# Kernel optimization log

Measured on AMD Instinct MI355X. Metric: run time of the kernel, lower is better.

## Reference

```python
import jax, jax.numpy as jnp
import numpy as np

D = 1024
B = 16
T = 2048
LN_EPS = 1e-5


def setup_inputs() -> dict:
    key = jax.random.key(0)
    k_x, k_in, k_st = jax.random.split(key, 3)
    x = jax.random.normal(k_x, (B, T, D), dtype=jnp.float32)
    # nn.Linear(d, 2d, bias=False): weight [2D, D], y = x @ W.T
    s_in = 1.0 / np.sqrt(D)
    W_in = jax.random.uniform(k_in, (2 * D, D), dtype=jnp.float32, minval=-s_in, maxval=s_in)
    W_state = jax.random.uniform(k_st, (D, D), dtype=jnp.float32, minval=-s_in, maxval=s_in)
    gamma = jnp.ones((D,), dtype=jnp.float32)
    beta = jnp.zeros((D,), dtype=jnp.float32)
    return {"x": x, "W_in": W_in, "W_state": W_state, "gamma": gamma, "beta": beta}


def _glru(x, W_in, W_state, gamma, beta):
    # Batched projections over all timesteps (gates depend only on x).
    proj = jnp.einsum("btd,ed->bte", x, W_in)            # [B, T, 2D]
    gx, vx = jnp.split(proj, 2, axis=-1)                   # each [B, T, D]
    u = jax.nn.sigmoid(gx)                                  # [B, T, D]
    cand = jnp.einsum("btd,ed->bte", vx, W_state)        # [B, T, D]

    # Sequential diagonal linear recurrence: h_t = u_t * h_{t-1} + (1-u_t)*cand_t
    def step(h, uc):
        u_t, c_t = uc
        h = u_t * h + (1.0 - u_t) * c_t
        return h, h

    h0 = jnp.zeros((x.shape[0], x.shape[2]), dtype=x.dtype)
    us = jnp.swapaxes(u, 0, 1)       # [T, B, D]
    cs = jnp.swapaxes(cand, 0, 1)    # [T, B, D]
    _, ys = jax.lax.scan(step, h0, (us, cs))
    y = jnp.swapaxes(ys, 0, 1)       # [B, T, D]

    # LayerNorm over last dim
    mu = jnp.mean(y, axis=-1, keepdims=True)
    var = jnp.mean(jnp.square(y - mu), axis=-1, keepdims=True)
    return (y - mu) * jax.lax.rsqrt(var + LN_EPS) * gamma + beta


def reference(x, W_in, W_state, gamma, beta):
    return _glru(x, W_in, W_state, gamma, beta)
```

## Files before the change

kernel.cpp:

```cpp
#include <hip/hip_runtime.h>

#define D_DIM 1024
#define B_DIM 16
#define T_DIM 2048
#define M_TOT (B_DIM * T_DIM)
#define K_DIM 1024
#define LN_EPS 1e-5f
#define CHUNK 16
#define NCH (T_DIM / CHUNK)

typedef _Float16 half8 __attribute__((ext_vector_type(8)));
typedef _Float16 half4v __attribute__((ext_vector_type(4)));
typedef float f32x4 __attribute__((ext_vector_type(4)));

__global__ __launch_bounds__(256) void prep_all(const float* __restrict__ x,
                                                const float* __restrict__ W_in,
                                                const float* __restrict__ W_state,
                                                _Float16* __restrict__ xh,
                                                _Float16* __restrict__ Wall,
                                                _Float16* __restrict__ wvxT,
                                                _Float16* __restrict__ wst) {
    __shared__ _Float16 t[32][33];
    int b = blockIdx.x, tid = threadIdx.x;
    if (b < 2048) {
        int i = b * 256 + tid;
        for (; i < M_TOT * K_DIM / 8; i += 2048 * 256) {
            const float4* p = (const float4*)x + 2 * (size_t)i;
            float4 a = p[0], c = p[1];
            half8 h;
            h[0] = (_Float16)a.x; h[1] = (_Float16)a.y; h[2] = (_Float16)a.z; h[3] = (_Float16)a.w;
            h[4] = (_Float16)c.x; h[5] = (_Float16)c.y; h[6] = (_Float16)c.z; h[7] = (_Float16)c.w;
            ((half8*)xh)[i] = h;
        }
    } else if (b < 2560) {
        int i = (b - 2048) * 256 + tid;
        const float4* p = (const float4*)W_in + 2 * (size_t)i;
        float4 a = p[0], c = p[1];
        half8 h;
        h[0] = (_Float16)a.x; h[1] = (_Float16)a.y; h[2] = (_Float16)a.z; h[3] = (_Float16)a.w;
        h[4] = (_Float16)c.x; h[5] = (_Float16)c.y; h[6] = (_Float16)c.z; h[7] = (_Float16)c.w;
        ((half8*)Wall)[i] = h;
    } else if (b < 3072) {
        int i = (b - 2560) * 256 + tid;
        const float4* p = (const float4*)W_state + 2 * (size_t)i;
        float4 a = p[0], c = p[1];
        half8 h;
        h[0] = (_Float16)a.x; h[1] = (_Float16)a.y; h[2] = (_Float16)a.z; h[3] = (_Float16)a.w;
        h[4] = (_Float16)c.x; h[5] = (_Float16)c.y; h[6] = (_Float16)c.z; h[7] = (_Float16)c.w;
        ((half8*)wst)[i] = h;
    } else {
        int tile = b - 3072;
        int bx = (tile & 31) * 32, by = (tile >> 5) * 32;
        int tx = tid & 31, ty = tid >> 5;
        const float* src = W_in + (size_t)D_DIM * K_DIM;
#pragma unroll
        for (int j = 0; j < 4; ++j)
            t[ty + 8 * j][tx] = (_Float16)src[(size_t)(by + ty + 8 * j) * 1024 + bx + tx];
        __syncthreads();
#pragma unroll
        for (int j = 0; j < 4; ++j)
            wvxT[(size_t)(bx + ty + 8 * j) * 1024 + by + tx] = t[tx][ty + 8 * j];
    }
}

__device__ __forceinline__ void gl_lds16(const _Float16* g, _Float16* l) {
    __builtin_amdgcn_global_load_lds(
        (const __attribute__((address_space(1))) unsigned int*)g,
        (__attribute__((address_space(3))) unsigned int*)l,
        16, 0, 0);
}


__device__ __forceinline__ void stageA32(const _Float16* __restrict__ G,
                                         int row0, int kt,
                                         _Float16* lds0, int wid, int lane) {
#pragma unroll
    for (int call = 0; call < 2; ++call) {
        int c0 = call * 256 + wid * 64;
        int c  = c0 + lane;
        int rl = c >> 2;
        int cc = c & 3;
        int src = cc ^ ((rl >> 1) & 3);
        gl_lds16(G + (size_t)(row0 + rl) * 1024 + kt + src * 8,
                 lds0 + (size_t)c0 * 8);
    }
}

__device__ __forceinline__ void stageB32(const _Float16* __restrict__ G,
                                         int nt, int kt,
                                         _Float16* lds0, int wid, int lane) {
#pragma unroll
    for (int call = 0; call < 4; ++call) {
        int c0 = call * 256 + wid * 64;
        int c  = c0 + lane;
        int rl = c >> 2;
        int cc = c & 3;
        int src = cc ^ ((rl >> 1) & 3);
        int row = nt * 128 + (rl & 127) + ((rl >> 7) << 10);
        gl_lds16(G + (size_t)row * 1024 + kt + src * 8,
                 lds0 + (size_t)c0 * 8);
    }
}

__device__ __forceinline__ half8 frag32(const _Float16* base, int row, int kq) {
    int cc = kq ^ ((row >> 1) & 3);
    return *(const half8*)(base + (size_t)row * 32 + cc * 8);
}

template <int TB>
__device__ __forceinline__ void gstep(const _Float16* __restrict__ A,
                                      const _Float16* __restrict__ W,
                                      int m0, int nt, int t, int nkt,
                                      int wid, int lane, int wc, int r, int kq,
                                      _Float16 (&As)[3][128][32],
                                      _Float16 (&Bs)[3][256][32],
                                      f32x4 (&acc)[8][4]) {
    constexpr int NB = (TB + 2) % 3;
    half8 rb[4], ra0[4], ra1[4];

    if (t + 1 < nkt) asm volatile("s_waitcnt vmcnt(6)" ::: "memory");
    else             asm volatile("s_waitcnt vmcnt(0)" ::: "memory");
    __builtin_amdgcn_s_barrier();
    __builtin_amdgcn_sched_barrier(0);

#pragma unroll
    for (int ni = 0; ni < 4; ni++)
        rb[ni] = frag32(&Bs[TB][0][0], (ni >> 1) * 128 + wc * 32 + (ni & 1) * 16 + r, kq);
#pragma unroll
    for (int mi = 0; mi < 4; mi++) ra0[mi] = frag32(&As[TB][0][0], mi * 16 + r, kq);
    if (t + 2 < nkt) {
        int kt2 = (t + 2) << 5;
        stageA32(A, m0, kt2, &As[NB][0][0], wid, lane);
        stageB32(W, nt, kt2, &Bs[NB][0][0], wid, lane);
    }
    __builtin_amdgcn_s_setprio(1);
#pragma unroll
    for (int mi = 0; mi < 4; mi++)
#pragma unroll
        for (int ni = 0; ni < 4; ni++)
            acc[mi][ni] = __builtin_amdgcn_mfma_f32_16x16x32_f16(ra0[mi], rb[ni], acc[mi][ni], 0, 0, 0);
    __builtin_amdgcn_s_setprio(0);

#pragma unroll
    for (int mi = 0; mi < 4; mi++) ra1[mi] = frag32(&As[TB][0][0], 64 + mi * 16 + r, kq);
    __builtin_amdgcn_s_setprio(1);
#pragma unroll
    for (int mi = 0; mi < 4; mi++)
#pragma unroll
        for (int ni = 0; ni < 4; ni++)
            acc[4 + mi][ni] = __builtin_amdgcn_mfma_f32_16x16x32_f16(ra1[mi], rb[ni], acc[4 + mi][ni], 0, 0, 0);
    __builtin_amdgcn_s_setprio(0);
    __builtin_amdgcn_s_barrier();
}

__global__ __launch_bounds__(256, 2) void gemm256(const _Float16* __restrict__ A,
                                                  const _Float16* __restrict__ W,
                                                  _Float16* __restrict__ out_u,
                                                  _Float16* __restrict__ out_c,
                                                  float* __restrict__ Ac,
                                                  float* __restrict__ Bc) {
    __shared__ _Float16 As[3][128][32];
    __shared__ _Float16 Bs[3][256][32];

    int bid = blockIdx.x;
    int xcd = bid & 7, lin = bid >> 3;
    int mt = xcd * 32 + (lin >> 3);
    int nt = lin & 7;
    int m0 = mt * 128;

    int tid = threadIdx.x, wid = tid >> 6, lane = tid & 63;
    int wc = wid;
    int r = lane & 15, kq = lane >> 4;

    f32x4 acc[8][4];
#pragma unroll
    for (int i = 0; i < 8; i++)
#pragma unroll
        for (int j = 0; j < 4; j++) acc[i][j] = (f32x4)0.f;

    const int nkt = K_DIM >> 5;

    stageA32(A, m0, 0,  &As[0][0][0], wid, lane);
    stageB32(W, nt, 0,  &Bs[0][0][0], wid, lane);
    stageA32(A, m0, 32, &As[1][0][0], wid, lane);
    stageB32(W, nt, 32, &Bs[1][0][0], wid, lane);

    for (int t0 = 0; t0 < nkt; t0 += 3) {
        gstep<0>(A, W, m0, nt, t0, nkt, wid, lane, wc, r, kq, As, Bs, acc);
        if (t0 + 1 < nkt)
            gstep<1>(A, W, m0, nt, t0 + 1, nkt, wid, lane, wc, r, kq, As, Bs, acc);
        if (t0 + 2 < nkt)
            gstep<2>(A, W, m0, nt, t0 + 2, nkt, wid, lane, wc, r, kq, As, Bs, acc);
    }

    int rr = kq * 4;
#pragma unroll
    for (int mi = 0; mi < 8; mi++) {
        int mbase = m0 + mi * 16 + rr;
        float Aab[2] = {1.f, 1.f}, Bab[2] = {0.f, 0.f};
#pragma unroll
        for (int ni = 0; ni < 2; ni++) {
            int d = nt * 128 + wc * 32 + ni * 16 + r;
#pragma unroll
            for (int q = 0; q < 4; q++) {
                float u = 1.f / (1.f + __expf(-acc[mi][ni][q]));
                float c = acc[mi][ni + 2][q];
                size_t m = (size_t)(mbase + q);
                out_u[m * D_DIM + d] = (_Float16)u;
                out_c[m * D_DIM + d] = (_Float16)c;
                Bab[ni] = fmaf(u, Bab[ni], (1.f - u) * c);
                Aab[ni] *= u;
            }
        }
#pragma unroll
        for (int ni = 0; ni < 2; ni++) {
            float Aa = Aab[ni], Bb = Bab[ni];
            float oA = __shfl_xor(Aa, 16), oB = __shfl_xor(Bb, 16);
            if (kq & 1) { Bb = fmaf(Aa, oB, Bb); Aa *= oA; }
            else        { Bb = fmaf(oA, Bb, oB); Aa *= oA; }
            oA = __shfl_xor(Aa, 32); oB = __shfl_xor(Bb, 32);
            if (kq & 2) { Bb = fmaf(Aa, oB, Bb); Aa *= oA; }
            else        { Bb = fmaf(oA, Bb, oB); Aa *= oA; }
            if (kq == 0) {
                int d = nt * 128 + wc * 32 + ni * 16 + r;
                int bc = mt * 8 + mi;
                Ac[(size_t)bc * 1024 + d] = Aa;
                Bc[(size_t)bc * 1024 + d] = Bb;
            }
        }
    }
}

__global__ __launch_bounds__(256) void wcomb_splitk(const _Float16* __restrict__ A,
                                                    const _Float16* __restrict__ Bm,
                                                    float* __restrict__ part) {
    __shared__ _Float16 As[128 * 32];
    __shared__ _Float16 Bs[128 * 32];
    int bid = blockIdx.x;
    int mt = bid & 7, nt = (bid >> 3) & 7, sl = bid >> 6;
    int m0 = mt * 128, n0 = nt * 128, kbeg = sl * 256;
    int tid = threadIdx.x, wid = tid >> 6, lane = tid & 63;
    int wr = wid >> 1, wc = wid & 1;

    f32x4 acc[4][4];
#pragma unroll
    for (int i = 0; i < 4; i++)
#pragma unroll
        for (int j = 0; j < 4; j++) acc[i][j] = (f32x4)0.f;

    int r = lane & 15, kq = lane >> 4;

    for (int kt = kbeg; kt < kbeg + 256; kt += 32) {
        __syncthreads();
#pragma unroll
        for (int j = 0; j < 2; ++j) {
            int f = j * 256 + tid;
            int row = f >> 2, kc = f & 3;
            gl_lds16(A + (size_t)(m0 + row) * 1024 + kt + kc * 8, As + (size_t)(j * 256 + wid * 64) * 8);
            gl_lds16(Bm + (size_t)(n0 + row) * 1024 + kt + kc * 8, Bs + (size_t)(j * 256 + wid * 64) * 8);
        }
        __syncthreads();
        half8 af[4], bf[4];
#pragma unroll
        for (int mi = 0; mi < 4; mi++) af[mi] = *(const half8*)&As[(wr * 64 + mi * 16 + r) * 32 + kq * 8];
#pragma unroll
        for (int ni = 0; ni < 4; ni++) bf[ni] = *(const half8*)&Bs[(wc * 64 + ni * 16 + r) * 32 + kq * 8];
#pragma unroll
        for (int mi = 0; mi < 4; mi++)
#pragma unroll
            for (int ni = 0; ni < 4; ni++)
                acc[mi][ni] = __builtin_amdgcn_mfma_f32_16x16x32_f16(af[mi], bf[ni], acc[mi][ni], 0, 0, 0);
    }

    int rr = kq * 4;
    float* pbp = part + (size_t)sl * 1048576;
#pragma unroll
    for (int mi = 0; mi < 4; mi++) {
        int mbase = m0 + wr * 64 + mi * 16 + rr;
#pragma unroll
        for (int ni = 0; ni < 4; ni++) {
            int n = n0 + wc * 64 + ni * 16 + r;
#pragma unroll
            for (int q = 0; q < 4; q++)
                pbp[(size_t)(mbase + q) * 1024 + n] = acc[mi][ni][q];
        }
    }
}

__global__ __launch_bounds__(256) void wcomb_combine(const float* __restrict__ part,
                                                     _Float16* __restrict__ out) {
    int i = blockIdx.x * 256 + threadIdx.x;
    float4 s0 = ((const float4*)part)[i];
    float4 s1 = ((const float4*)(part + 1048576))[i];
    float4 s2 = ((const float4*)(part + 2097152))[i];
    float4 s3 = ((const float4*)(part + 3145728))[i];
    half4v o;
    o[0] = (_Float16)(s0.x + s1.x + s2.x + s3.x);
    o[1] = (_Float16)(s0.y + s1.y + s2.y + s3.y);
    o[2] = (_Float16)(s0.z + s1.z + s2.z + s3.z);
    o[3] = (_Float16)(s0.w + s1.w + s2.w + s3.w);
    ((half4v*)out)[i] = o;
}

__global__ __launch_bounds__(256) void scan_pass2(float* __restrict__ AcH0,
                                                  const float* __restrict__ Bc) {
    int idx = blockIdx.x * 256 + threadIdx.x;
    int b = idx >> 10, d = idx & (D_DIM - 1);
    float h = 0.f;
#pragma unroll 8
    for (int ch = 0; ch < NCH; ++ch) {
        size_t k = ((size_t)(b * NCH + ch) << 10) + d;
        float a = AcH0[k];
        float bv = Bc[k];
        AcH0[k] = h;
        h = fmaf(a, h, bv);
    }
}

__global__ __launch_bounds__(64) void scan_ln(const _Float16* __restrict__ u,
                                              const _Float16* __restrict__ cd,
                                              const float* __restrict__ h0,
                                              const float* __restrict__ gamma,
                                              const float* __restrict__ beta,
                                              float* __restrict__ outp) {
    int bc = blockIdx.x;
    int b = bc >> 7, ch = bc & (NCH - 1);
    int lane = threadIdx.x;
    int d0 = lane * 16;
    size_t base = ((size_t)b * T_DIM + (size_t)ch * CHUNK) * D_DIM + d0;

    float g[16], be[16], h[16];
#pragma unroll
    for (int j = 0; j < 16; j += 4) {
        *(float4*)&g[j]  = *(const float4*)&gamma[d0 + j];
        *(float4*)&be[j] = *(const float4*)&beta[d0 + j];
    }
    size_t o = (size_t)bc * D_DIM + d0;
#pragma unroll
    for (int j = 0; j < 16; j += 4) *(float4*)&h[j] = *(const float4*)&h0[o + j];

    for (int t = 0; t < CHUNK; ++t) {
        size_t row = base + (size_t)t * D_DIM;
        half8 ua = *(const half8*)&u[row];
        half8 ub = *(const half8*)&u[row + 8];
        half8 ca = *(const half8*)&cd[row];
        half8 cb = *(const half8*)&cd[row + 8];
        float s = 0.f, q = 0.f;
#pragma unroll
        for (int j = 0; j < 8; ++j) {
            float ut = (float)ua[j], ct = (float)ca[j];
            h[j] = fmaf(ut, h[j] - ct, ct);
            s += h[j]; q += h[j] * h[j];
        }
#pragma unroll
        for (int j = 0; j < 8; ++j) {
            float ut = (float)ub[j], ct = (float)cb[j];
            h[8 + j] = fmaf(ut, h[8 + j] - ct, ct);
            s += h[8 + j]; q += h[8 + j] * h[8 + j];
        }
#pragma unroll
        for (int off = 32; off > 0; off >>= 1) {
            s += __shfl_xor(s, off);
            q += __shfl_xor(q, off);
        }
        float mu = s * (1.f / D_DIM);
        float var = q * (1.f / D_DIM) - mu * mu;
        float rs = rsqrtf(var + LN_EPS);
        float o16[16];
#pragma unroll
        for (int j = 0; j < 16; ++j) o16[j] = (h[j] - mu) * rs * g[j] + be[j];
#pragma unroll
        for (int j = 0; j < 16; j += 4) *(float4*)&outp[row + j] = *(float4*)&o16[j];
    }
}

extern "C" void kernel_launch(void* const* d_in, const int* in_sizes, int n_in,
                              void* d_out, int out_size, void* d_ws, size_t ws_size,
                              hipStream_t stream) {
    const float* x       = (const float*)d_in[0];
    const float* W_in    = (const float*)d_in[1];
    const float* W_state = (const float*)d_in[2];
    const float* gamma   = (const float*)d_in[3];
    const float* beta    = (const float*)d_in[4];
    float* out = (float*)d_out;

    char* w = (char*)d_ws;
    size_t off = 0;
    auto carve = [&](size_t bytes) {
        void* p = w + off;
        off += (bytes + 255) & ~(size_t)255;
        return p;
    };
    _Float16* xh   = (_Float16*)carve((size_t)M_TOT * K_DIM * 2);
    _Float16* Wall = (_Float16*)carve((size_t)2 * D_DIM * K_DIM * 2);
    _Float16* uarr = (_Float16*)carve((size_t)M_TOT * D_DIM * 2);
    _Float16* cand = (_Float16*)carve((size_t)M_TOT * D_DIM * 2);
    char* scratch  = (char*)carve((size_t)16 * 1024 * 1024);
    _Float16* wvxT = (_Float16*)scratch;
    _Float16* wst  = (_Float16*)(scratch + 2 * 1024 * 1024);
    float* Ac = (float*)scratch;
    float* Bc = (float*)(scratch + 8 * 1024 * 1024);
    float* wpart = (float*)cand;

    prep_all<<<4096, 256, 0, stream>>>(x, W_in, W_state, xh, Wall, wvxT, wst);

    wcomb_splitk<<<256, 256, 0, stream>>>(wst, wvxT, wpart);
    wcomb_combine<<<1024, 256, 0, stream>>>(wpart, Wall + (size_t)D_DIM * K_DIM);

    gemm256<<<2048, 256, 0, stream>>>(xh, Wall, uarr, cand, Ac, Bc);

    scan_pass2<<<(B_DIM * D_DIM) / 256, 256, 0, stream>>>(Ac, Bc);
    scan_ln<<<B_DIM * NCH, 64, 0, stream>>>(uarr, cand, Ac, gamma, beta, out);
}
```

Before: 300.9 us.

## Pre-pack GEMM weights in MFMA fragment order and load B directly to registers

Weights are repacked, in prep_all and in a new fused combine-and-pack kernel, into a fragment-major layout matching the MFMA B operand. Each wave then loads its B fragments straight from global memory into registers, one k-step ahead, instead of staging the B tile through LDS. This removes the B-side LDS buffers and LDS reads, which shrinks shared memory per block and cuts LDS traffic. In exchange, the register-prefetched B loads are issued only one step ahead, so global and L2 latency may be exposed right before the MFMAs.

Result: no change. 301.1 us (+0.1%).

```diff
diff --git a/kernel.cpp b/kernel.cpp
--- a/kernel.cpp
+++ b/kernel.cpp
@@ -13,11 +13,12 @@
 typedef _Float16 half4v __attribute__((ext_vector_type(4)));
 typedef float f32x4 __attribute__((ext_vector_type(4)));
 
+
 __global__ __launch_bounds__(256) void prep_all(const float* __restrict__ x,
                                                 const float* __restrict__ W_in,
                                                 const float* __restrict__ W_state,
                                                 _Float16* __restrict__ xh,
-                                                _Float16* __restrict__ Wall,
+                                                _Float16* __restrict__ pk,
                                                 _Float16* __restrict__ wvxT,
                                                 _Float16* __restrict__ wst) {
     __shared__ _Float16 t[32][33];
@@ -34,12 +35,16 @@
         }
     } else if (b < 2560) {
         int i = (b - 2048) * 256 + tid;
-        const float4* p = (const float4*)W_in + 2 * (size_t)i;
-        float4 a = p[0], c = p[1];
+        int ll = i & 63, u = i >> 6;
+        int kt = u & 31, nf = u >> 5;
+        int n = nf * 16 + (ll & 15);
+        int k = kt * 32 + (ll >> 4) * 8;
+        const float4* s = (const float4*)&W_in[(size_t)n * 1024 + k];
+        float4 a = s[0], c = s[1];
         half8 h;
         h[0] = (_Float16)a.x; h[1] = (_Float16)a.y; h[2] = (_Float16)a.z; h[3] = (_Float16)a.w;
         h[4] = (_Float16)c.x; h[5] = (_Float16)c.y; h[6] = (_Float16)c.z; h[7] = (_Float16)c.w;
-        ((half8*)Wall)[i] = h;
+        *(half8*)&pk[(size_t)i * 8] = h;
     } else if (b < 3072) {
         int i = (b - 2560) * 256 + tid;
         const float4* p = (const float4*)W_state + 2 * (size_t)i;
@@ -86,37 +91,25 @@
     }
 }
 
-__device__ __forceinline__ void stageB32(const _Float16* __restrict__ G,
-                                         int nt, int kt,
-                                         _Float16* lds0, int wid, int lane) {
-#pragma unroll
-    for (int call = 0; call < 4; ++call) {
-        int c0 = call * 256 + wid * 64;
-        int c  = c0 + lane;
-        int rl = c >> 2;
-        int cc = c & 3;
-        int src = cc ^ ((rl >> 1) & 3);
-        int row = nt * 128 + (rl & 127) + ((rl >> 7) << 10);
-        gl_lds16(G + (size_t)row * 1024 + kt + src * 8,
-                 lds0 + (size_t)c0 * 8);
-    }
-}
-
 __device__ __forceinline__ half8 frag32(const _Float16* base, int row, int kq) {
     int cc = kq ^ ((row >> 1) & 3);
     return *(const half8*)(base + (size_t)row * 32 + cc * 8);
 }
 
-template <int TB>
+__device__ __forceinline__ half8 bload(const _Float16* __restrict__ pb,
+                                       int nf, int kt, int lane) {
+    return *(const half8*)(pb + (((size_t)nf * 32 + kt) * 64 + lane) * 8);
+}
+
+template <int TA>
 __device__ __forceinline__ void gstep(const _Float16* __restrict__ A,
-                                      const _Float16* __restrict__ W,
-                                      int m0, int nt, int t, int nkt,
-                                      int wid, int lane, int wc, int r, int kq,
+                                      const _Float16* __restrict__ pb,
+                                      int m0, int nf0, int t, int nkt,
+                                      int wid, int lane, int r, int kq,
                                       _Float16 (&As)[3][128][32],
-                                      _Float16 (&Bs)[3][256][32],
+                                      half8 (&bb)[4],
                                       f32x4 (&acc)[8][4]) {
-    constexpr int NB = (TB + 2) % 3;
-    half8 rb[4], ra0[4], ra1[4];
+    half8 ra0[4], ra1[4];
 
     if (t + 1 < nkt) asm volatile("s_waitcnt vmcnt(6)" ::: "memory");
     else             asm volatile("s_waitcnt vmcnt(0)" ::: "memory");
@@ -124,43 +117,41 @@
     __builtin_amdgcn_sched_barrier(0);
 
 #pragma unroll
-    for (int ni = 0; ni < 4; ni++)
-        rb[ni] = frag32(&Bs[TB][0][0], (ni >> 1) * 128 + wc * 32 + (ni & 1) * 16 + r, kq);
-#pragma unroll
-    for (int mi = 0; mi < 4; mi++) ra0[mi] = frag32(&As[TB][0][0], mi * 16 + r, kq);
-    if (t + 2 < nkt) {
-        int kt2 = (t + 2) << 5;
-        stageA32(A, m0, kt2, &As[NB][0][0], wid, lane);
-        stageB32(W, nt, kt2, &Bs[NB][0][0], wid, lane);
-    }
+    for (int mi = 0; mi < 4; mi++) ra0[mi] = frag32(&As[TA][0][0], mi * 16 + r, kq);
+    if (t + 2 < nkt) stageA32(A, m0, (t + 2) << 5, &As[(TA + 2) % 3][0][0], wid, lane);
     __builtin_amdgcn_s_setprio(1);
 #pragma unroll
     for (int mi = 0; mi < 4; mi++)
 #pragma unroll
         for (int ni = 0; ni < 4; ni++)
-            acc[mi][ni] = __builtin_amdgcn_mfma_f32_16x16x32_f16(ra0[mi], rb[ni], acc[mi][ni], 0, 0, 0);
+            acc[mi][ni] = __builtin_amdgcn_mfma_f32_16x16x32_f16(ra0[mi], bb[ni], acc[mi][ni], 0, 0, 0);
     __builtin_amdgcn_s_setprio(0);
 
 #pragma unroll
-    for (int mi = 0; mi < 4; mi++) ra1[mi] = frag32(&As[TB][0][0], 64 + mi * 16 + r, kq);
+    for (int mi = 0; mi < 4; mi++) ra1[mi] = frag32(&As[TA][0][0], 64 + mi * 16 + r, kq);
     __builtin_amdgcn_s_setprio(1);
 #pragma unroll
     for (int mi = 0; mi < 4; mi++)
 #pragma unroll
         for (int ni = 0; ni < 4; ni++)
-            acc[4 + mi][ni] = __builtin_amdgcn_mfma_f32_16x16x32_f16(ra1[mi], rb[ni], acc[4 + mi][ni], 0, 0, 0);
+            acc[4 + mi][ni] = __builtin_amdgcn_mfma_f32_16x16x32_f16(ra1[mi], bb[ni], acc[4 + mi][ni], 0, 0, 0);
     __builtin_amdgcn_s_setprio(0);
+    if (t + 1 < nkt) {
+        bb[0] = bload(pb, nf0,      t + 1, lane);
+        bb[1] = bload(pb, nf0 + 1,  t + 1, lane);
+        bb[2] = bload(pb, nf0 + 64, t + 1, lane);
+        bb[3] = bload(pb, nf0 + 65, t + 1, lane);
+    }
     __builtin_amdgcn_s_barrier();
 }
 
 __global__ __launch_bounds__(256, 2) void gemm256(const _Float16* __restrict__ A,
-                                                  const _Float16* __restrict__ W,
+                                                  const _Float16* __restrict__ pk,
                                                   _Float16* __restrict__ out_u,
                                                   _Float16* __restrict__ out_c,
                                                   float* __restrict__ Ac,
                                                   float* __restrict__ Bc) {
     __shared__ _Float16 As[3][128][32];
-    __shared__ _Float16 Bs[3][256][32];
 
     int bid = blockIdx.x;
     int xcd = bid & 7, lin = bid >> 3;
@@ -171,6 +162,7 @@
     int tid = threadIdx.x, wid = tid >> 6, lane = tid & 63;
     int wc = wid;
     int r = lane & 15, kq = lane >> 4;
+    int nf0 = nt * 8 + wc * 2;
 
     f32x4 acc[8][4];
 #pragma unroll
@@ -178,19 +170,22 @@
 #pragma unroll
         for (int j = 0; j < 4; j++) acc[i][j] = (f32x4)0.f;
 
+    half8 bb[4];
     const int nkt = K_DIM >> 5;
 
     stageA32(A, m0, 0,  &As[0][0][0], wid, lane);
-    stageB32(W, nt, 0,  &Bs[0][0][0], wid, lane);
     stageA32(A, m0, 32, &As[1][0][0], wid, lane);
-    stageB32(W, nt, 32, &Bs[1][0][0], wid, lane);
+    bb[0] = bload(pk, nf0,      0, lane);
+    bb[1] = bload(pk, nf0 + 1,  0, lane);
+    bb[2] = bload(pk, nf0 + 64, 0, lane);
+    bb[3] = bload(pk, nf0 + 65, 0, lane);
 
     for (int t0 = 0; t0 < nkt; t0 += 3) {
-        gstep<0>(A, W, m0, nt, t0, nkt, wid, lane, wc, r, kq, As, Bs, acc);
+        gstep<0>(A, pk, m0, nf0, t0, nkt, wid, lane, r, kq, As, bb, acc);
         if (t0 + 1 < nkt)
-            gstep<1>(A, W, m0, nt, t0 + 1, nkt, wid, lane, wc, r, kq, As, Bs, acc);
+            gstep<1>(A, pk, m0, nf0, t0 + 1, nkt, wid, lane, r, kq, As, bb, acc);
         if (t0 + 2 < nkt)
-            gstep<2>(A, W, m0, nt, t0 + 2, nkt, wid, lane, wc, r, kq, As, Bs, acc);
+            gstep<2>(A, pk, m0, nf0, t0 + 2, nkt, wid, lane, r, kq, As, bb, acc);
     }
 
     int rr = kq * 4;
@@ -287,19 +282,28 @@
     }
 }
 
-__global__ __launch_bounds__(256) void wcomb_combine(const float* __restrict__ part,
-                                                     _Float16* __restrict__ out) {
+__global__ __launch_bounds__(256) void wcomb_combine_pack(const float* __restrict__ part,
+                                                          _Float16* __restrict__ pk) {
     int i = blockIdx.x * 256 + threadIdx.x;
-    float4 s0 = ((const float4*)part)[i];
-    float4 s1 = ((const float4*)(part + 1048576))[i];
-    float4 s2 = ((const float4*)(part + 2097152))[i];
-    float4 s3 = ((const float4*)(part + 3145728))[i];
-    half4v o;
-    o[0] = (_Float16)(s0.x + s1.x + s2.x + s3.x);
-    o[1] = (_Float16)(s0.y + s1.y + s2.y + s3.y);
-    o[2] = (_Float16)(s0.z + s1.z + s2.z + s3.z);
-    o[3] = (_Float16)(s0.w + s1.w + s2.w + s3.w);
-    ((half4v*)out)[i] = o;
+    int ll = i & 63, u = i >> 6;
+    int kt = u & 31, nf = u >> 5;
+    int e = nf * 16 + (ll & 15);
+    int k = kt * 32 + (ll >> 4) * 8;
+    size_t o = (size_t)e * 1024 + k;
+    float s[8];
+#pragma unroll
+    for (int j = 0; j < 8; ++j) s[j] = 0.f;
+#pragma unroll
+    for (int sl = 0; sl < 4; ++sl) {
+        const float4* p = (const float4*)&part[(size_t)sl * 1048576 + o];
+        float4 a = p[0], c = p[1];
+        s[0] += a.x; s[1] += a.y; s[2] += a.z; s[3] += a.w;
+        s[4] += c.x; s[5] += c.y; s[6] += c.z; s[7] += c.w;
+    }
+    half8 h;
+#pragma unroll
+    for (int j = 0; j < 8; ++j) h[j] = (_Float16)s[j];
+    *(half8*)&pk[1048576 + (size_t)i * 8] = h;
 }
 
 __global__ __launch_bounds__(256) void scan_pass2(float* __restrict__ AcH0,
@@ -392,7 +396,7 @@
         return p;
     };
     _Float16* xh   = (_Float16*)carve((size_t)M_TOT * K_DIM * 2);
-    _Float16* Wall = (_Float16*)carve((size_t)2 * D_DIM * K_DIM * 2);
+    _Float16* pk   = (_Float16*)carve((size_t)2 * D_DIM * K_DIM * 2);
     _Float16* uarr = (_Float16*)carve((size_t)M_TOT * D_DIM * 2);
     _Float16* cand = (_Float16*)carve((size_t)M_TOT * D_DIM * 2);
     char* scratch  = (char*)carve((size_t)16 * 1024 * 1024);
@@ -402,12 +406,12 @@
     float* Bc = (float*)(scratch + 8 * 1024 * 1024);
     float* wpart = (float*)cand;
 
-    prep_all<<<4096, 256, 0, stream>>>(x, W_in, W_state, xh, Wall, wvxT, wst);
+    prep_all<<<4096, 256, 0, stream>>>(x, W_in, W_state, xh, pk, wvxT, wst);
 
     wcomb_splitk<<<256, 256, 0, stream>>>(wst, wvxT, wpart);
-    wcomb_combine<<<1024, 256, 0, stream>>>(wpart, Wall + (size_t)D_DIM * K_DIM);
-
-    gemm256<<<2048, 256, 0, stream>>>(xh, Wall, uarr, cand, Ac, Bc);
+    wcomb_combine_pack<<<512, 256, 0, stream>>>(wpart, pk);
+
+    gemm256<<<2048, 256, 0, stream>>>(xh, pk, uarr, cand, Ac, Bc);
 
     scan_pass2<<<(B_DIM * D_DIM) / 256, 256, 0, stream>>>(Ac, Bc);
     scan_ln<<<B_DIM * NCH, 64, 0, stream>>>(uarr, cand, Ac, gamma, beta, out);
```
